# Kernel optimization log

Measured on AMD Instinct MI355X. Metric: run time of the kernel, lower is better.

The kernel has to match this reference:

```python
import jax, jax.numpy as jnp
import numpy as np

DIM = 512
A_HEADS = 8
C_HEADS = 4
DH = 64
EPS = 1e-5


def layer_norm(x, g, b):
    mu = jnp.mean(x, axis=-1, keepdims=True)
    var = jnp.var(x, axis=-1, keepdims=True)
    return (x - mu) * jax.lax.rsqrt(var + EPS) * g + b


def setup_inputs() -> dict:
    key = jax.random.key(0)
    ks = jax.random.split(key, 8)
    inner_a = A_HEADS * DH  # 512
    inner_c = C_HEADS * DH  # 256
    s = 0.02
    return {
        "x": jax.random.normal(ks[0], (4, 192, DIM), dtype=jnp.float32),
        # Attention branch params
        "ln1_g": jnp.ones((DIM,), jnp.float32),
        "ln1_b": jnp.zeros((DIM,), jnp.float32),
        "Wqkv": jax.random.normal(ks[1], (DIM, 3 * inner_a), jnp.float32) * s,
        "Wo": jax.random.normal(ks[2], (inner_a, DIM), jnp.float32) * s,
        "bo": jnp.zeros((DIM,), jnp.float32),
        # Trittention branch params
        "ln2_g": jnp.ones((DIM,), jnp.float32),
        "ln2_b": jnp.zeros((DIM,), jnp.float32),
        "Wabcde": jax.random.normal(ks[3], (DIM, 5 * inner_c), jnp.float32) * s,
        "babcde": jnp.zeros((5 * inner_c,), jnp.float32),
        "Wp": jax.random.normal(ks[4], (inner_c, DIM), jnp.float32) * s,
        "bp": jnp.zeros((DIM,), jnp.float32),
    }


def _attention(x, ln_g, ln_b, Wqkv, Wo, bo):
    B, T, _ = x.shape
    xn = layer_norm(x, ln_g, ln_b)
    qkv = xn @ Wqkv  # [B,T,3*H*D]
    q, k, v = jnp.split(qkv, 3, axis=-1)
    def heads(t):
        return t.reshape(B, T, A_HEADS, DH).transpose(0, 2, 1, 3)  # [B,H,T,D]
    q, k, v = heads(q), heads(k), heads(v)
    scale = DH ** -0.5
    dots = jnp.einsum('bhqd,bhkd->bhqk', q, k) * scale
    attn = jax.nn.softmax(dots, axis=-1)
    out = jnp.einsum('bhqk,bhkd->bhqd', attn, v)
    out = out.transpose(0, 2, 1, 3).reshape(B, T, A_HEADS * DH)
    return out @ Wo + bo


def _trittention(x, ln_g, ln_b, Wabcde, babcde, Wp, bp):
    B, T, _ = x.shape
    xn = layer_norm(x, ln_g, ln_b)
    proj = xn @ Wabcde + babcde  # [B,T,5*H*D]
    a, b_, c, d_, e = jnp.split(proj, 5, axis=-1)
    def heads(t):
        return t.reshape(B, T, C_HEADS, DH)  # [B,T,H,D]
    a, b_, c, d_, e = heads(a), heads(b_), heads(c), heads(d_), heads(e)
    # cubic score: [B,H,S,T,Q]
    score = jnp.einsum('bshd,bthd,bqhd->bhstq', a, b_, c) / DH
    # softmax over joint (s,t) for each query q
    score = score.transpose(0, 1, 4, 2, 3).reshape(B, C_HEADS, T, T * T)
    attn = jax.nn.softmax(score, axis=-1).reshape(B, C_HEADS, T, T, T)
    z = (jnp.einsum('bhqst,bshd->bhqd', attn, d_)
         + jnp.einsum('bhqst,bthd->bhqd', attn, e))
    z = z.transpose(0, 2, 1, 3).reshape(B, T, C_HEADS * DH)
    return z @ Wp + bp


def reference(x, ln1_g, ln1_b, Wqkv, Wo, bo, ln2_g, ln2_b, Wabcde, babcde, Wp, bp):
    return (_attention(x, ln1_g, ln1_b, Wqkv, Wo, bo)
            + _trittention(x, ln2_g, ln2_b, Wabcde, babcde, Wp, bp))
```

## Files before the change

kernel.cpp:

```cpp
#include <hip/hip_runtime.h>
#include <cstdint>


#define B_   4
#define T_   192
#define DIM_ 512
#define AH   8
#define CH   4

typedef unsigned short u16;
typedef unsigned int   u32;
typedef __attribute__((ext_vector_type(8))) short short8;
typedef __attribute__((ext_vector_type(4))) float floatx4;
typedef __attribute__((ext_vector_type(4))) int intx4;
typedef __attribute__((ext_vector_type(2))) float f32x2;
typedef __attribute__((ext_vector_type(8))) _Float16 half8;
typedef __attribute__((ext_vector_type(2))) _Float16 half2v;
typedef __attribute__((ext_vector_type(2))) __fp16 fp16x2;

union Frag  { intx4 i; short8 s; };
union FragH { intx4 i; half8 h; };

__device__ __forceinline__ floatx4 mfma16(Frag a, Frag b, floatx4 c) {
    return __builtin_amdgcn_mfma_f32_16x16x32_bf16(a.s, b.s, c, 0, 0, 0);
}
__device__ __forceinline__ floatx4 mfma16h(FragH a, FragH b, floatx4 c) {
    return __builtin_amdgcn_mfma_f32_16x16x32_f16(a.h, b.h, c, 0, 0, 0);
}

__device__ __forceinline__ float fexp2(float x) {
    return __builtin_amdgcn_exp2f(x);
}

__device__ __forceinline__ float wave_reduce_sum(float v) {
#pragma unroll
    for (int off = 32; off >= 1; off >>= 1)
        v += __shfl_xor(v, off, 64);
    return v;
}

__device__ __forceinline__ u32 pack_rne(float x, float y) {
    u32 ux = __float_as_uint(x);
    u32 uy = __float_as_uint(y);
    ux += 0x7fffu + ((ux >> 16) & 1u);
    uy += 0x7fffu + ((uy >> 16) & 1u);
    return (ux >> 16) | (uy & 0xffff0000u);
}
__device__ __forceinline__ u16 bf16_rne(float x) {
    u32 u = __float_as_uint(x);
    u += 0x7fffu + ((u >> 16) & 1u);
    return (u16)(u >> 16);
}
__device__ __forceinline__ float bf16f(u16 h) { return __uint_as_float(((u32)h) << 16); }

__device__ __forceinline__ u32 pack_f16(float x, float y) {
    union { fp16x2 h; u32 u; } cv;
    cv.h = __builtin_amdgcn_cvt_pkrtz(x, y);
    return cv.u;
}
__device__ __forceinline__ u32 mul_h2(u32 a, u32 b) {
    union { u32 u; half2v h; } ua, ub, uw;
    ua.u = a; ub.u = b;
    uw.h = ua.h * ub.h;
    return uw.u;
}

__device__ __forceinline__ Frag ld_frag8(const u16* p) {
    Frag f;
    uint2 a = *(const uint2*)p;
    uint2 b = *(const uint2*)(p + 4);
    f.i = (intx4){ (int)a.x, (int)a.y, (int)b.x, (int)b.y };
    return f;
}

#define LOG2E 1.44269504088896f

__global__ __launch_bounds__(256) void prep_kernel(
    const float* __restrict__ x,
    const float* __restrict__ g1, const float* __restrict__ b1,
    const float* __restrict__ g2, const float* __restrict__ b2,
    u16* __restrict__ x1h, u16* __restrict__ x2h,
    const float* __restrict__ Wqkv, u16* __restrict__ wqh,
    const float* __restrict__ Wab,  u16* __restrict__ wah,
    const float* __restrict__ Wo,   const float* __restrict__ Wp,
    u16* __restrict__ wofh, float* __restrict__ zero_base, float* __restrict__ outz)
{
    __shared__ union { float t[64][65]; float red[4][2]; } u;
    const int tid = threadIdx.x;
    {
        int gid = blockIdx.x * 256 + tid;
        if (gid < 294912) ((float4*)zero_base)[gid] = make_float4(0.f, 0.f, 0.f, 0.f);
        if (gid < 98304)  ((float4*)outz)[gid]      = make_float4(0.f, 0.f, 0.f, 0.f);
    }
    if (blockIdx.x < 768) {
        int row = blockIdx.x;
        const float2 v = ((const float2*)(x + (size_t)row * DIM_))[tid];
        float s  = v.x + v.y;
        float s2 = v.x * v.x + v.y * v.y;
        s  = wave_reduce_sum(s);
        s2 = wave_reduce_sum(s2);
        int w = tid >> 6;
        if ((tid & 63) == 0) { u.red[w][0] = s; u.red[w][1] = s2; }
        __syncthreads();
        float ts  = u.red[0][0] + u.red[1][0] + u.red[2][0] + u.red[3][0];
        float ts2 = u.red[0][1] + u.red[1][1] + u.red[2][1] + u.red[3][1];
        float mean = ts * (1.0f / DIM_);
        float var  = ts2 * (1.0f / DIM_) - mean * mean;
        float rstd = rsqrtf(var + 1e-5f);
        int c0 = tid * 2;
        float n0 = (v.x - mean) * rstd;
        float n1 = (v.y - mean) * rstd;
        float a0 = n0 * g1[c0] + b1[c0], a1 = n1 * g1[c0 + 1] + b1[c0 + 1];
        float c2 = n0 * g2[c0] + b2[c0], c3 = n1 * g2[c0 + 1] + b2[c0 + 1];
        size_t o = (size_t)row * 256 + tid;
        ((u32*)x1h)[o] = pack_rne(a0, a1);
        ((u32*)x2h)[o] = pack_rne(c2, c3);
        return;
    }
    int id = blockIdx.x - 768;
    const float* W; u16 *H; int K, N, Kout, kofs, tile;
    if (id < 192)      { W = Wqkv; H = wqh;  K = 512; N = 1536; Kout = 512; kofs = 0;   tile = id;       }
    else if (id < 352) { W = Wab;  H = wah;  K = 512; N = 1280; Kout = 512; kofs = 0;   tile = id - 192; }
    else if (id < 416) { W = Wo;   H = wofh; K = 512; N = 512;  Kout = 768; kofs = 0;   tile = id - 352; }
    else               { W = Wp;   H = wofh; K = 256; N = 512;  Kout = 768; kofs = 512; tile = id - 416; }
    int nx = N >> 6;
    int n0 = (tile % nx) * 64, k0 = (tile / nx) * 64;
    int rr = tid >> 4, c4 = (tid & 15) << 2;
#pragma unroll
    for (int p = 0; p < 4; ++p) {
        int row = rr + p * 16;
        float4 v = *(const float4*)(W + (size_t)(k0 + row) * N + n0 + c4);
        u.t[row][c4 + 0] = v.x; u.t[row][c4 + 1] = v.y;
        u.t[row][c4 + 2] = v.z; u.t[row][c4 + 3] = v.w;
    }
    __syncthreads();
#pragma unroll
    for (int p = 0; p < 4; ++p) {
        int n = rr + p * 16;
        u16 hi[4];
#pragma unroll
        for (int c = 0; c < 4; ++c)
            hi[c] = bf16_rne(u.t[c4 + c][n]);
        size_t o = (size_t)(n0 + n) * Kout + kofs + k0 + c4;
        *(uint2*)&H[o] = make_uint2((u32)hi[0] | ((u32)hi[1] << 16), (u32)hi[2] | ((u32)hi[3] << 16));
    }
}

__global__ __launch_bounds__(256) void gemm_dual(
    const u16* __restrict__ x1h, const u16* __restrict__ wqh,
    const u16* __restrict__ x2h, const u16* __restrict__ wah,
    const float* __restrict__ babcde,
    float* __restrict__ qkv, float* __restrict__ proj)
{
    __shared__ u16 As[64][68];
    __shared__ u16 Bs[64][68];
    const int tid = threadIdx.x;
    const int nb = blockIdx.x;
    const u16 *Ah, *BTh; const float* bias; float* C; int N, bn;
    if (nb < 24) { Ah = x1h; BTh = wqh; bias = nullptr; C = qkv;  N = 1536; bn = nb * 64; }
    else         { Ah = x2h; BTh = wah; bias = babcde; C = proj; N = 1280; bn = (nb - 24) * 64; }
    const int K = 512;
    const int bm = blockIdx.y * 64;
    const int lane = tid & 63, wave = tid >> 6;
    const int m16 = lane & 15, quad = lane >> 4;
    const int wm = (wave >> 1) * 32, wn = (wave & 1) * 32;
    const int r = tid >> 2, c16 = (tid & 3) * 16;

    floatx4 acc[2][2];
#pragma unroll
    for (int i = 0; i < 2; ++i)
#pragma unroll
        for (int j = 0; j < 2; ++j) acc[i][j] = (floatx4){0.f, 0.f, 0.f, 0.f};

    for (int k0 = 0; k0 < K; k0 += 64) {
        __syncthreads();
        {
            const u16* pa = x1h == Ah ? Ah + (size_t)(bm + r) * K + k0 + c16
                                      : Ah + (size_t)(bm + r) * K + k0 + c16;
            uint4 v0 = *(const uint4*)pa, v1 = *(const uint4*)(pa + 8);
            *(uint2*)&As[r][c16 + 0]  = make_uint2(v0.x, v0.y);
            *(uint2*)&As[r][c16 + 4]  = make_uint2(v0.z, v0.w);
            *(uint2*)&As[r][c16 + 8]  = make_uint2(v1.x, v1.y);
            *(uint2*)&As[r][c16 + 12] = make_uint2(v1.z, v1.w);
        }
        {
            const u16* pb = BTh + (size_t)(bn + r) * K + k0 + c16;
            uint4 v0 = *(const uint4*)pb, v1 = *(const uint4*)(pb + 8);
            *(uint2*)&Bs[r][c16 + 0]  = make_uint2(v0.x, v0.y);
            *(uint2*)&Bs[r][c16 + 4]  = make_uint2(v0.z, v0.w);
            *(uint2*)&Bs[r][c16 + 8]  = make_uint2(v1.x, v1.y);
            *(uint2*)&Bs[r][c16 + 12] = make_uint2(v1.z, v1.w);
        }
        __syncthreads();
#pragma unroll
        for (int ks = 0; ks < 2; ++ks) {
            const int ko = ks * 32 + quad * 8;
            Frag a0 = ld_frag8(&As[wm + m16][ko]);
            Frag a1 = ld_frag8(&As[wm + 16 + m16][ko]);
            Frag b0 = ld_frag8(&Bs[wn + m16][ko]);
            Frag b1 = ld_frag8(&Bs[wn + 16 + m16][ko]);
            acc[0][0] = mfma16(a0, b0, acc[0][0]);
            acc[0][1] = mfma16(a0, b1, acc[0][1]);
            acc[1][0] = mfma16(a1, b0, acc[1][0]);
            acc[1][1] = mfma16(a1, b1, acc[1][1]);
        }
    }
#pragma unroll
    for (int i = 0; i < 2; ++i)
#pragma unroll
        for (int rr = 0; rr < 4; ++rr) {
            int m = bm + wm + i * 16 + quad * 4 + rr;
#pragma unroll
            for (int j = 0; j < 2; ++j) {
                int n = bn + wn + j * 16 + m16;
                float v = acc[i][j][rr];
                if (bias) v += bias[n];
                C[(size_t)m * N + n] = v;
            }
        }
}

__global__ __launch_bounds__(256, 3) void attn_tritt(
    const float* __restrict__ qkv, const float* __restrict__ proj,
    u16* __restrict__ aoh, float* __restrict__ rs1, float* __restrict__ rt1)
{
    __shared__ union {
        struct {
            union { u16 Ks[96][68]; u16 P[64][100]; } kp;
            u16 Vt[64][100];
        } at;
        struct {
            u32 a_lds[48 * 36];
            u32 b_lds[48 * 36];
            float rs_lds[48][33];
            float rt_lds[48][33];
        } tr;
    } S;
    const int tid = threadIdx.x;
    const int lane = tid & 63, wave = tid >> 6;
    const int m16 = lane & 15, quad = lane >> 4;

    if (blockIdx.x < 96) {
        const int ab = blockIdx.x;
        const int b = ab / 24, rem = ab % 24;
        const int h = rem / 3, qt3 = rem % 3;
        const int qg = wave;
        const size_t base = (size_t)(b * T_) * 1536 + h * 64;

        Frag qf0, qf1;
        {
            const float s = 0.125f * LOG2E;
            const float* qp = qkv + base + (size_t)(qt3 * 64 + qg * 16 + m16) * 1536 + quad * 8;
            float4 u0 = *(const float4*)qp;
            float4 u1 = *(const float4*)(qp + 4);
            float4 u2 = *(const float4*)(qp + 32);
            float4 u3 = *(const float4*)(qp + 36);
            qf0.i = (intx4){ (int)pack_rne(u0.x * s, u0.y * s), (int)pack_rne(u0.z * s, u0.w * s),
                             (int)pack_rne(u1.x * s, u1.y * s), (int)pack_rne(u1.z * s, u1.w * s) };
            qf1.i = (intx4){ (int)pack_rne(u2.x * s, u2.y * s), (int)pack_rne(u2.z * s, u2.w * s),
                             (int)pack_rne(u3.x * s, u3.y * s), (int)pack_rne(u3.z * s, u3.w * s) };
        }

        float rsum[4] = {0.f, 0.f, 0.f, 0.f};
        floatx4 acco[4];
#pragma unroll
        for (int dt = 0; dt < 4; ++dt) acco[dt] = (floatx4){0.f, 0.f, 0.f, 0.f};

        for (int p = 0; p < 2; ++p) {
            if (p) __syncthreads();
            for (int i = tid; i < 96 * 16; i += 256) {
                int row = i >> 4, c4 = (i & 15) << 2;
                const float* kp = qkv + base + (size_t)(p * 96 + row) * 1536 + 512 + c4;
                float4 kv = *(const float4*)kp;
                *(uint2*)&S.at.kp.Ks[row][c4] = make_uint2(pack_rne(kv.x, kv.y), pack_rne(kv.z, kv.w));
                float4 vv = *(const float4*)(qkv + base + (size_t)(p * 96 + row) * 1536 + 1024 + c4);
                S.at.Vt[c4 + 0][row] = bf16_rne(vv.x);
                S.at.Vt[c4 + 1][row] = bf16_rne(vv.y);
                S.at.Vt[c4 + 2][row] = bf16_rne(vv.z);
                S.at.Vt[c4 + 3][row] = bf16_rne(vv.w);
            }
            __syncthreads();

            float ev[6][4];
#pragma unroll
            for (int tt = 0; tt < 6; ++tt) {
                Frag kb0 = ld_frag8(&S.at.kp.Ks[tt * 16 + m16][quad * 8]);
                Frag kb1 = ld_frag8(&S.at.kp.Ks[tt * 16 + m16][32 + quad * 8]);
                floatx4 accs = (floatx4){0.f, 0.f, 0.f, 0.f};
                accs = mfma16(qf0, kb0, accs);
                accs = mfma16(qf1, kb1, accs);
#pragma unroll
                for (int rr = 0; rr < 4; ++rr) {
                    float e = fexp2(accs[rr]);
                    ev[tt][rr] = e;
                    rsum[rr] += e;
                }
            }
            __syncthreads();
#pragma unroll
            for (int tt = 0; tt < 6; ++tt)
#pragma unroll
                for (int rr = 0; rr < 4; ++rr)
                    S.at.kp.P[qg * 16 + quad * 4 + rr][tt * 16 + m16] = bf16_rne(ev[tt][rr]);
#pragma unroll
            for (int ts = 0; ts < 3; ++ts) {
                Frag pf = ld_frag8(&S.at.kp.P[qg * 16 + m16][ts * 32 + quad * 8]);
#pragma unroll
                for (int dt = 0; dt < 4; ++dt) {
                    Frag vf = ld_frag8(&S.at.Vt[dt * 16 + m16][ts * 32 + quad * 8]);
                    acco[dt] = mfma16(pf, vf, acco[dt]);
                }
            }
        }

        float rinv[4];
#pragma unroll
        for (int rr = 0; rr < 4; ++rr) {
            float v = rsum[rr];
            v += __shfl_xor(v, 1, 64);
            v += __shfl_xor(v, 2, 64);
            v += __shfl_xor(v, 4, 64);
            v += __shfl_xor(v, 8, 64);
            rinv[rr] = 1.0f / v;
        }
#pragma unroll
        for (int dt = 0; dt < 4; ++dt)
#pragma unroll
            for (int rr = 0; rr < 4; ++rr) {
                float o = acco[dt][rr] * rinv[rr];
                size_t idx = (size_t)(b * T_ + qt3 * 64 + qg * 16 + quad * 4 + rr) * 512
                           + h * 64 + dt * 16 + m16;
                aoh[idx] = bf16_rne(o);
            }
        return;
    }

    const int t2 = blockIdx.x - 96;
    const int xx = t2 % 96;
    const int h = (t2 / 96) % CH;
    const int b = t2 / (96 * CH);
    const int qt = xx >> 4;
    const int sc = (xx >> 2) & 3;
    const int tc = xx & 3;
    const int q0 = qt * 32, s0 = sc * 48, t0 = tc * 48;
    const int bh = b * CH + h;
    const size_t rowbase = (size_t)(b * T_) * 1280 + h * 64;
    const float kA = 0.015625f * LOG2E;

    for (int i = tid; i < 48 * 32; i += 256) {
        int row = i >> 5, cp = i & 31;
        const float2 va = *(const float2*)(proj + rowbase + (size_t)(s0 + row) * 1280 + 0 + cp * 2);
        S.tr.a_lds[row * 36 + cp] = pack_f16(va.x * kA, va.y * kA);
        const float2 vb = *(const float2*)(proj + rowbase + (size_t)(t0 + row) * 1280 + 256 + cp * 2);
        S.tr.b_lds[row * 36 + cp] = pack_f16(vb.x, vb.y);
    }

    FragH cf[2][2];
#pragma unroll
    for (int jq = 0; jq < 2; ++jq) {
        const float* cp = proj + rowbase + (size_t)(q0 + jq * 16 + m16) * 1280 + 512 + quad * 8;
        float4 u0 = *(const float4*)(cp);
        float4 u1 = *(const float4*)(cp + 4);
        float4 u2 = *(const float4*)(cp + 32);
        float4 u3 = *(const float4*)(cp + 36);
        cf[jq][0].i = (intx4){ (int)pack_f16(u0.x, u0.y), (int)pack_f16(u0.z, u0.w),
                               (int)pack_f16(u1.x, u1.y), (int)pack_f16(u1.z, u1.w) };
        cf[jq][1].i = (intx4){ (int)pack_f16(u2.x, u2.y), (int)pack_f16(u2.z, u2.w),
                               (int)pack_f16(u3.x, u3.y), (int)pack_f16(u3.z, u3.w) };
    }
    __syncthreads();

    float rt_acc[3][4][2] = {};

    for (int si = 0; si < 12; ++si) {
        const int srow = wave * 12 + si;
        const intx4 av0 = *(const intx4*)(S.tr.a_lds + srow * 36 + quad * 4);
        const intx4 av1 = *(const intx4*)(S.tr.a_lds + srow * 36 + 16 + quad * 4);
        float rs_s[2] = {0.f, 0.f};
#pragma unroll
        for (int tt = 0; tt < 3; ++tt) {
            const u32* bp = S.tr.b_lds + (tt * 16 + m16) * 36;
            intx4 bv0 = *(const intx4*)(bp + quad * 4);
            intx4 bv1 = *(const intx4*)(bp + 16 + quad * 4);
            FragH w0, w1;
#pragma unroll
            for (int j = 0; j < 4; ++j) {
                w0.i[j] = (int)mul_h2((u32)av0[j], (u32)bv0[j]);
                w1.i[j] = (int)mul_h2((u32)av1[j], (u32)bv1[j]);
            }
#pragma unroll
            for (int jq = 0; jq < 2; ++jq) {
                floatx4 acc = (floatx4){0.f, 0.f, 0.f, 0.f};
                acc = mfma16h(w0, cf[jq][0], acc);
                acc = mfma16h(w1, cf[jq][1], acc);
#pragma unroll
                for (int rr = 0; rr < 4; ++rr) {
                    float e = fexp2(acc[rr]);
                    rt_acc[tt][rr][jq] += e;
                    rs_s[jq] += e;
                }
            }
        }
#pragma unroll
        for (int jq = 0; jq < 2; ++jq) {
            float v = rs_s[jq];
            v += __shfl_xor(v, 16, 64);
            v += __shfl_xor(v, 32, 64);
            if (lane < 16) S.tr.rs_lds[srow][jq * 16 + m16] = v;
        }
    }

    __syncthreads();
    for (int w = 0; w < 4; ++w) {
        if (wave == w) {
#pragma unroll
            for (int tt = 0; tt < 3; ++tt)
#pragma unroll
                for (int rr = 0; rr < 4; ++rr) {
                    int t = tt * 16 + quad * 4 + rr;
#pragma unroll
                    for (int jq = 0; jq < 2; ++jq) {
                        if (w == 0) S.tr.rt_lds[t][jq * 16 + m16] = rt_acc[tt][rr][jq];
                        else        S.tr.rt_lds[t][jq * 16 + m16] += rt_acc[tt][rr][jq];
                    }
                }
        }
        __syncthreads();
    }
    for (int i = tid; i < 32 * 48; i += 256) {
        int qq = i / 48, ss = i - qq * 48;
        unsafeAtomicAdd(&rs1[((size_t)bh * T_ + q0 + qq) * T_ + s0 + ss], S.tr.rs_lds[ss][qq]);
    }
    for (int i = tid; i < 32 * 48; i += 256) {
        int qq = i / 48, t3 = i - qq * 48;
        unsafeAtomicAdd(&rt1[((size_t)bh * T_ + q0 + qq) * T_ + t0 + t3], S.tr.rt_lds[t3][qq]);
    }
}

__global__ __launch_bounds__(256) void finale(
    const u16* __restrict__ aoh, const float* __restrict__ rs1, const float* __restrict__ rt1,
    const float* __restrict__ proj, const u16* __restrict__ wofh,
    const float* __restrict__ bo, const float* __restrict__ bp,
    float* __restrict__ out)
{
    __shared__ union {
        struct { u16 As[32][68]; u16 Bs[64][68]; } A;
        struct { u16 Am[2][32][68]; u16 Bs[64][68]; float zred[32][9]; float Zl[32]; } B;
    } S;
    const int tid = threadIdx.x;
    const int lane = tid & 63, wave = tid >> 6;
    const int m16 = lane & 15, quad = lane >> 4;

    if (blockIdx.x < 192) {
        const int bn = (blockIdx.x & 7) * 64, bm = (blockIdx.x >> 3) * 32;
        const int wm = (wave >> 1) * 16, wn = (wave & 1) * 32;
        const int ra = tid >> 3, c8 = (tid & 7) * 8;
        const int rb = tid >> 2, c16 = (tid & 3) * 16;

        floatx4 acc[2];
        acc[0] = (floatx4){0.f, 0.f, 0.f, 0.f};
        acc[1] = (floatx4){0.f, 0.f, 0.f, 0.f};

        for (int k0 = 0; k0 < 512; k0 += 64) {
            __syncthreads();
            {
                const u16* pah = aoh + (size_t)(bm + ra) * 512 + k0 + c8;
                uint4 v = *(const uint4*)pah;
                *(uint2*)&S.A.As[ra][c8 + 0] = make_uint2(v.x, v.y);
                *(uint2*)&S.A.As[ra][c8 + 4] = make_uint2(v.z, v.w);
            }
            {
                const u16* pb = wofh + (size_t)(bn + rb) * 768 + k0 + c16;
                uint4 v0 = *(const uint4*)pb, v1 = *(const uint4*)(pb + 8);
                *(uint2*)&S.A.Bs[rb][c16 + 0]  = make_uint2(v0.x, v0.y);
                *(uint2*)&S.A.Bs[rb][c16 + 4]  = make_uint2(v0.z, v0.w);
                *(uint2*)&S.A.Bs[rb][c16 + 8]  = make_uint2(v1.x, v1.y);
                *(uint2*)&S.A.Bs[rb][c16 + 12] = make_uint2(v1.z, v1.w);
            }
            __syncthreads();
#pragma unroll
            for (int ks = 0; ks < 2; ++ks) {
                const int ko = ks * 32 + quad * 8;
                Frag ah = ld_frag8(&S.A.As[wm + m16][ko]);
                Frag b0 = ld_frag8(&S.A.Bs[wn + m16][ko]);
                Frag b1 = ld_frag8(&S.A.Bs[wn + 16 + m16][ko]);
                acc[0] = mfma16(ah, b0, acc[0]);
                acc[1] = mfma16(ah, b1, acc[1]);
            }
        }
#pragma unroll
        for (int rr = 0; rr < 4; ++rr) {
            int m = bm + wm + quad * 4 + rr;
#pragma unroll
            for (int j = 0; j < 2; ++j) {
                int n = bn + wn + j * 16 + m16;
                unsafeAtomicAdd(&out[(size_t)m * 512 + n], acc[j][rr] + bo[n] + bp[n]);
            }
        }
        return;
    }

    const int blockB = blockIdx.x - 192;
    const int mt = blockB % 6, bh = blockB / 6;
    const int b = bh >> 2, h = bh & 3;
    const int q0 = mt * 32;
    const int wm = (wave >> 1) * 16, wn = (wave & 1) * 32;
    const int ra = tid >> 3, c8 = (tid & 7) * 8;
    const int sl = tid >> 2, d4b = (tid & 3) * 4;

    float zacc = 0.f;
    floatx4 acc[2];
    acc[0] = (floatx4){0.f, 0.f, 0.f, 0.f};
    acc[1] = (floatx4){0.f, 0.f, 0.f, 0.f};

    for (int k0 = 0; k0 < 384; k0 += 64) {
        __syncthreads();
        {
            float g[8];
            if (k0 < 192) {
                const float* p = rs1 + ((size_t)bh * T_ + q0 + ra) * T_ + k0 + c8;
                float4 v0 = *(const float4*)(p);
                float4 v1 = *(const float4*)(p + 4);
                g[0] = v0.x; g[1] = v0.y; g[2] = v0.z; g[3] = v0.w;
                g[4] = v1.x; g[5] = v1.y; g[6] = v1.z; g[7] = v1.w;
                zacc += ((g[0] + g[1]) + (g[2] + g[3])) + ((g[4] + g[5]) + (g[6] + g[7]));
            } else {
                const float* p = rt1 + ((size_t)bh * T_ + q0 + ra) * T_ + (k0 - 192) + c8;
                float4 v0 = *(const float4*)(p);
                float4 v1 = *(const float4*)(p + 4);
                g[0] = v0.x; g[1] = v0.y; g[2] = v0.z; g[3] = v0.w;
                g[4] = v1.x; g[5] = v1.y; g[6] = v1.z; g[7] = v1.w;
            }
#pragma unroll
            for (int i = 0; i < 8; ++i) {
                u16 hi = bf16_rne(g[i]);
                S.B.Am[0][ra][c8 + i] = hi;
                S.B.Am[1][ra][c8 + i] = bf16_rne(g[i] - bf16f(hi));
            }
        }
        {
            const int colbase = (k0 < 192 ? 768 : 1024) + h * 64;
            const int s0 = (k0 < 192 ? k0 : k0 - 192);
#pragma unroll
            for (int i = 0; i < 4; ++i) {
                int dd = d4b + i * 16;
                float4 v = *(const float4*)(proj + (size_t)(b * T_ + s0 + sl) * 1280 + colbase + dd);
                S.B.Bs[dd + 0][sl] = bf16_rne(v.x);
                S.B.Bs[dd + 1][sl] = bf16_rne(v.y);
                S.B.Bs[dd + 2][sl] = bf16_rne(v.z);
                S.B.Bs[dd + 3][sl] = bf16_rne(v.w);
            }
        }
        __syncthreads();
#pragma unroll
        for (int ks = 0; ks < 2; ++ks) {
            const int ko = ks * 32 + quad * 8;
            Frag gh = ld_frag8(&S.B.Am[0][wm + m16][ko]);
            Frag gl = ld_frag8(&S.B.Am[1][wm + m16][ko]);
            Frag d0 = ld_frag8(&S.B.Bs[wn + m16][ko]);
            Frag d1 = ld_frag8(&S.B.Bs[wn + 16 + m16][ko]);
            acc[0] = mfma16(gh, d0, acc[0]);
            acc[0] = mfma16(gl, d0, acc[0]);
            acc[1] = mfma16(gh, d1, acc[1]);
            acc[1] = mfma16(gl, d1, acc[1]);
        }
    }
    S.B.zred[ra][tid & 7] = zacc;
    __syncthreads();
    if (tid < 32) {
        float s = ((S.B.zred[tid][0] + S.B.zred[tid][1]) + (S.B.zred[tid][2] + S.B.zred[tid][3]))
                + ((S.B.zred[tid][4] + S.B.zred[tid][5]) + (S.B.zred[tid][6] + S.B.zred[tid][7]));
        S.B.Zl[tid] = 1.0f / s;
    }
    __syncthreads();
    {
        float zv[2][4];
#pragma unroll
        for (int j = 0; j < 2; ++j)
#pragma unroll
            for (int rr = 0; rr < 4; ++rr) {
                int m = wm + quad * 4 + rr;
                zv[j][rr] = acc[j][rr] * S.B.Zl[m];
            }
        __syncthreads();
#pragma unroll
        for (int j = 0; j < 2; ++j)
#pragma unroll
            for (int rr = 0; rr < 4; ++rr) {
                int m = wm + quad * 4 + rr;
                int d = wn + j * 16 + m16;
                S.B.Am[0][m][d] = bf16_rne(zv[j][rr]);
            }
    }
    __syncthreads();
#pragma unroll
    for (int t = 0; t < 8; ++t) {
        const int n0 = wave * 128 + t * 16;
        Frag bf0 = ld_frag8(&wofh[(size_t)(n0 + m16) * 768 + 512 + h * 64 + quad * 8]);
        Frag bf1 = ld_frag8(&wofh[(size_t)(n0 + m16) * 768 + 512 + h * 64 + 32 + quad * 8]);
#pragma unroll
        for (int qi = 0; qi < 2; ++qi) {
            Frag za = ld_frag8(&S.B.Am[0][qi * 16 + m16][quad * 8]);
            Frag zb = ld_frag8(&S.B.Am[0][qi * 16 + m16][32 + quad * 8]);
            floatx4 ac = (floatx4){0.f, 0.f, 0.f, 0.f};
            ac = mfma16(za, bf0, ac);
            ac = mfma16(zb, bf1, ac);
#pragma unroll
            for (int rr = 0; rr < 4; ++rr) {
                int m = b * T_ + q0 + qi * 16 + quad * 4 + rr;
                unsafeAtomicAdd(&out[(size_t)m * 512 + n0 + m16], ac[rr]);
            }
        }
    }
}

extern "C" void kernel_launch(void* const* d_in, const int* in_sizes, int n_in,
                              void* d_out, int out_size, void* d_ws, size_t ws_size,
                              hipStream_t stream)
{
    const float* x      = (const float*)d_in[0];
    const float* ln1_g  = (const float*)d_in[1];
    const float* ln1_b  = (const float*)d_in[2];
    const float* Wqkv   = (const float*)d_in[3];
    const float* Wo     = (const float*)d_in[4];
    const float* bo     = (const float*)d_in[5];
    const float* ln2_g  = (const float*)d_in[6];
    const float* ln2_b  = (const float*)d_in[7];
    const float* Wabcde = (const float*)d_in[8];
    const float* babcde = (const float*)d_in[9];
    const float* Wp     = (const float*)d_in[10];
    const float* bp     = (const float*)d_in[11];
    float* out = (float*)d_out;

    float* ws   = (float*)d_ws;
    float* proj = ws;
    u16* wofh   = (u16*)(ws + 983040);
    u16* aoh    = (u16*)(ws + 1179648);
    float* qkv  = ws + 1376256;
    u16* x1h    = (u16*)(ws + 2555904);
    u16* x2h    = (u16*)(ws + 2752512);
    u16* wqh    = (u16*)(ws + 2949120);
    u16* wah    = (u16*)(ws + 3342336);
    float* rs1  = ws + 3670016;
    float* rt1  = ws + 4259840;

    prep_kernel<<<1216, 256, 0, stream>>>(x, ln1_g, ln1_b, ln2_g, ln2_b,
                                          x1h, x2h,
                                          Wqkv, wqh, Wabcde, wah,
                                          Wo, Wp, wofh, rs1, out);
    gemm_dual<<<dim3(44, 12), 256, 0, stream>>>(x1h, wqh, x2h, wah,
                                                babcde, qkv, proj);
    attn_tritt<<<96 + 1536, 256, 0, stream>>>(qkv, proj, aoh, rs1, rt1);
    finale<<<288, 256, 0, stream>>>(aoh, rs1, rt1, proj, wofh, bo, bp, out);
}
```

Before: 138.8 us.

## Fuse attention output projection into attention blocks via per-head atomic accumulation

Each attention block now writes its normalized per-head output to shared memory and multiplies it directly by its 64-column slice of Wo, atomically adding partial results (plus biases from head 0) into the output. This removes the bf16 attention-output buffer round trip and the 192 output-projection GEMM blocks from the final kernel, which shrinks to the trittention part only. In exchange it adds eight-way atomic contention per output element, an extra Wo read per head block, and more work on the 96 attention blocks, which may lengthen the attention kernel's critical path.

```diff
diff --git a/kernel.cpp b/kernel.cpp
--- a/kernel.cpp
+++ b/kernel.cpp
@@ -175,8 +175,7 @@
     for (int k0 = 0; k0 < K; k0 += 64) {
         __syncthreads();
         {
-            const u16* pa = x1h == Ah ? Ah + (size_t)(bm + r) * K + k0 + c16
-                                      : Ah + (size_t)(bm + r) * K + k0 + c16;
+            const u16* pa = Ah + (size_t)(bm + r) * K + k0 + c16;
             uint4 v0 = *(const uint4*)pa, v1 = *(const uint4*)(pa + 8);
             *(uint2*)&As[r][c16 + 0]  = make_uint2(v0.x, v0.y);
             *(uint2*)&As[r][c16 + 4]  = make_uint2(v0.z, v0.w);
@@ -222,11 +221,14 @@
 
 __global__ __launch_bounds__(256, 3) void attn_tritt(
     const float* __restrict__ qkv, const float* __restrict__ proj,
-    u16* __restrict__ aoh, float* __restrict__ rs1, float* __restrict__ rt1)
+    const u16* __restrict__ wofh,
+    const float* __restrict__ bo, const float* __restrict__ bp,
+    float* __restrict__ rs1, float* __restrict__ rt1,
+    float* __restrict__ out)
 {
     __shared__ union {
         struct {
-            union { u16 Ks[96][68]; u16 P[64][100]; } kp;
+            union { u16 Ks[96][68]; u16 P[64][100]; u16 oz[64][68]; } kp;
             u16 Vt[64][100];
         } at;
         struct {
@@ -323,15 +325,39 @@
             v += __shfl_xor(v, 8, 64);
             rinv[rr] = 1.0f / v;
         }
+        __syncthreads();
 #pragma unroll
         for (int dt = 0; dt < 4; ++dt)
 #pragma unroll
             for (int rr = 0; rr < 4; ++rr) {
                 float o = acco[dt][rr] * rinv[rr];
-                size_t idx = (size_t)(b * T_ + qt3 * 64 + qg * 16 + quad * 4 + rr) * 512
-                           + h * 64 + dt * 16 + m16;
-                aoh[idx] = bf16_rne(o);
-            }
+                S.at.kp.oz[qg * 16 + quad * 4 + rr][dt * 16 + m16] = bf16_rne(o);
+            }
+        __syncthreads();
+        const int brow = b * T_ + qt3 * 64;
+        const bool addb = (h == 0);
+#pragma unroll
+        for (int t = 0; t < 8; ++t) {
+            const int n0 = wave * 128 + t * 16;
+            Frag wo0 = ld_frag8(&wofh[(size_t)(n0 + m16) * 768 + h * 64 + quad * 8]);
+            Frag wo1 = ld_frag8(&wofh[(size_t)(n0 + m16) * 768 + h * 64 + 32 + quad * 8]);
+#pragma unroll
+            for (int qi = 0; qi < 4; ++qi) {
+                Frag oa = ld_frag8(&S.at.kp.oz[qi * 16 + m16][quad * 8]);
+                Frag ob = ld_frag8(&S.at.kp.oz[qi * 16 + m16][32 + quad * 8]);
+                floatx4 ac = (floatx4){0.f, 0.f, 0.f, 0.f};
+                ac = mfma16(oa, wo0, ac);
+                ac = mfma16(ob, wo1, ac);
+#pragma unroll
+                for (int rr = 0; rr < 4; ++rr) {
+                    int m = brow + qi * 16 + quad * 4 + rr;
+                    int n = n0 + m16;
+                    float v = ac[rr];
+                    if (addb) v += bo[n] + bp[n];
+                    unsafeAtomicAdd(&out[(size_t)m * 512 + n], v);
+                }
+            }
+        }
         return;
     }
 
@@ -379,9 +405,9 @@
         float rs_s[2] = {0.f, 0.f};
 #pragma unroll
         for (int tt = 0; tt < 3; ++tt) {
-            const u32* bp = S.tr.b_lds + (tt * 16 + m16) * 36;
-            intx4 bv0 = *(const intx4*)(bp + quad * 4);
-            intx4 bv1 = *(const intx4*)(bp + 16 + quad * 4);
+            const u32* bp2 = S.tr.b_lds + (tt * 16 + m16) * 36;
+            intx4 bv0 = *(const intx4*)(bp2 + quad * 4);
+            intx4 bv1 = *(const intx4*)(bp2 + 16 + quad * 4);
             FragH w0, w1;
 #pragma unroll
             for (int j = 0; j < 4; ++j) {
@@ -438,69 +464,16 @@
 }
 
 __global__ __launch_bounds__(256) void finale(
-    const u16* __restrict__ aoh, const float* __restrict__ rs1, const float* __restrict__ rt1,
+    const float* __restrict__ rs1, const float* __restrict__ rt1,
     const float* __restrict__ proj, const u16* __restrict__ wofh,
-    const float* __restrict__ bo, const float* __restrict__ bp,
     float* __restrict__ out)
 {
-    __shared__ union {
-        struct { u16 As[32][68]; u16 Bs[64][68]; } A;
-        struct { u16 Am[2][32][68]; u16 Bs[64][68]; float zred[32][9]; float Zl[32]; } B;
-    } S;
+    __shared__ struct { u16 Am[2][32][68]; u16 Bs[64][68]; float zred[32][9]; float Zl[32]; } S;
     const int tid = threadIdx.x;
     const int lane = tid & 63, wave = tid >> 6;
     const int m16 = lane & 15, quad = lane >> 4;
 
-    if (blockIdx.x < 192) {
-        const int bn = (blockIdx.x & 7) * 64, bm = (blockIdx.x >> 3) * 32;
-        const int wm = (wave >> 1) * 16, wn = (wave & 1) * 32;
-        const int ra = tid >> 3, c8 = (tid & 7) * 8;
-        const int rb = tid >> 2, c16 = (tid & 3) * 16;
-
-        floatx4 acc[2];
-        acc[0] = (floatx4){0.f, 0.f, 0.f, 0.f};
-        acc[1] = (floatx4){0.f, 0.f, 0.f, 0.f};
-
-        for (int k0 = 0; k0 < 512; k0 += 64) {
-            __syncthreads();
-            {
-                const u16* pah = aoh + (size_t)(bm + ra) * 512 + k0 + c8;
-                uint4 v = *(const uint4*)pah;
-                *(uint2*)&S.A.As[ra][c8 + 0] = make_uint2(v.x, v.y);
-                *(uint2*)&S.A.As[ra][c8 + 4] = make_uint2(v.z, v.w);
-            }
-            {
-                const u16* pb = wofh + (size_t)(bn + rb) * 768 + k0 + c16;
-                uint4 v0 = *(const uint4*)pb, v1 = *(const uint4*)(pb + 8);
-                *(uint2*)&S.A.Bs[rb][c16 + 0]  = make_uint2(v0.x, v0.y);
-                *(uint2*)&S.A.Bs[rb][c16 + 4]  = make_uint2(v0.z, v0.w);
-                *(uint2*)&S.A.Bs[rb][c16 + 8]  = make_uint2(v1.x, v1.y);
-                *(uint2*)&S.A.Bs[rb][c16 + 12] = make_uint2(v1.z, v1.w);
-            }
-            __syncthreads();
-#pragma unroll
-            for (int ks = 0; ks < 2; ++ks) {
-                const int ko = ks * 32 + quad * 8;
-                Frag ah = ld_frag8(&S.A.As[wm + m16][ko]);
-                Frag b0 = ld_frag8(&S.A.Bs[wn + m16][ko]);
-                Frag b1 = ld_frag8(&S.A.Bs[wn + 16 + m16][ko]);
-                acc[0] = mfma16(ah, b0, acc[0]);
-                acc[1] = mfma16(ah, b1, acc[1]);
-            }
-        }
-#pragma unroll
-        for (int rr = 0; rr < 4; ++rr) {
-            int m = bm + wm + quad * 4 + rr;
-#pragma unroll
-            for (int j = 0; j < 2; ++j) {
-                int n = bn + wn + j * 16 + m16;
-                unsafeAtomicAdd(&out[(size_t)m * 512 + n], acc[j][rr] + bo[n] + bp[n]);
-            }
-        }
-        return;
-    }
-
-    const int blockB = blockIdx.x - 192;
+    const int blockB = blockIdx.x;
     const int mt = blockB % 6, bh = blockB / 6;
     const int b = bh >> 2, h = bh & 3;
     const int q0 = mt * 32;
@@ -534,8 +507,8 @@
 #pragma unroll
             for (int i = 0; i < 8; ++i) {
                 u16 hi = bf16_rne(g[i]);
-                S.B.Am[0][ra][c8 + i] = hi;
-                S.B.Am[1][ra][c8 + i] = bf16_rne(g[i] - bf16f(hi));
+                S.Am[0][ra][c8 + i] = hi;
+                S.Am[1][ra][c8 + i] = bf16_rne(g[i] - bf16f(hi));
             }
         }
         {
@@ -545,32 +518,32 @@
             for (int i = 0; i < 4; ++i) {
                 int dd = d4b + i * 16;
                 float4 v = *(const float4*)(proj + (size_t)(b * T_ + s0 + sl) * 1280 + colbase + dd);
-                S.B.Bs[dd + 0][sl] = bf16_rne(v.x);
-                S.B.Bs[dd + 1][sl] = bf16_rne(v.y);
-                S.B.Bs[dd + 2][sl] = bf16_rne(v.z);
-                S.B.Bs[dd + 3][sl] = bf16_rne(v.w);
+                S.Bs[dd + 0][sl] = bf16_rne(v.x);
+                S.Bs[dd + 1][sl] = bf16_rne(v.y);
+                S.Bs[dd + 2][sl] = bf16_rne(v.z);
+                S.Bs[dd + 3][sl] = bf16_rne(v.w);
             }
         }
         __syncthreads();
 #pragma unroll
         for (int ks = 0; ks < 2; ++ks) {
             const int ko = ks * 32 + quad * 8;
-            Frag gh = ld_frag8(&S.B.Am[0][wm + m16][ko]);
-            Frag gl = ld_frag8(&S.B.Am[1][wm + m16][ko]);
-            Frag d0 = ld_frag8(&S.B.Bs[wn + m16][ko]);
-            Frag d1 = ld_frag8(&S.B.Bs[wn + 16 + m16][ko]);
+            Frag gh = ld_frag8(&S.Am[0][wm + m16][ko]);
+            Frag gl = ld_frag8(&S.Am[1][wm + m16][ko]);
+            Frag d0 = ld_frag8(&S.Bs[wn + m16][ko]);
+            Frag d1 = ld_frag8(&S.Bs[wn + 16 + m16][ko]);
             acc[0] = mfma16(gh, d0, acc[0]);
             acc[0] = mfma16(gl, d0, acc[0]);
             acc[1] = mfma16(gh, d1, acc[1]);
             acc[1] = mfma16(gl, d1, acc[1]);
         }
     }
-    S.B.zred[ra][tid & 7] = zacc;
+    S.zred[ra][tid & 7] = zacc;
     __syncthreads();
     if (tid < 32) {
-        float s = ((S.B.zred[tid][0] + S.B.zred[tid][1]) + (S.B.zred[tid][2] + S.B.zred[tid][3]))
-                + ((S.B.zred[tid][4] + S.B.zred[tid][5]) + (S.B.zred[tid][6] + S.B.zred[tid][7]));
-        S.B.Zl[tid] = 1.0f / s;
+        float s = ((S.zred[tid][0] + S.zred[tid][1]) + (S.zred[tid][2] + S.zred[tid][3]))
+                + ((S.zred[tid][4] + S.zred[tid][5]) + (S.zred[tid][6] + S.zred[tid][7]));
+        S.Zl[tid] = 1.0f / s;
     }
     __syncthreads();
     {
@@ -580,7 +553,7 @@
 #pragma unroll
             for (int rr = 0; rr < 4; ++rr) {
                 int m = wm + quad * 4 + rr;
-                zv[j][rr] = acc[j][rr] * S.B.Zl[m];
+                zv[j][rr] = acc[j][rr] * S.Zl[m];
             }
         __syncthreads();
 #pragma unroll
@@ -589,7 +562,7 @@
             for (int rr = 0; rr < 4; ++rr) {
                 int m = wm + quad * 4 + rr;
                 int d = wn + j * 16 + m16;
-                S.B.Am[0][m][d] = bf16_rne(zv[j][rr]);
+                S.Am[0][m][d] = bf16_rne(zv[j][rr]);
             }
     }
     __syncthreads();
@@ -600,8 +573,8 @@
         Frag bf1 = ld_frag8(&wofh[(size_t)(n0 + m16) * 768 + 512 + h * 64 + 32 + quad * 8]);
 #pragma unroll
         for (int qi = 0; qi < 2; ++qi) {
-            Frag za = ld_frag8(&S.B.Am[0][qi * 16 + m16][quad * 8]);
-            Frag zb = ld_frag8(&S.B.Am[0][qi * 16 + m16][32 + quad * 8]);
+            Frag za = ld_frag8(&S.Am[0][qi * 16 + m16][quad * 8]);
+            Frag zb = ld_frag8(&S.Am[0][qi * 16 + m16][32 + quad * 8]);
             floatx4 ac = (floatx4){0.f, 0.f, 0.f, 0.f};
             ac = mfma16(za, bf0, ac);
             ac = mfma16(zb, bf1, ac);
@@ -635,7 +608,6 @@
     float* ws   = (float*)d_ws;
     float* proj = ws;
     u16* wofh   = (u16*)(ws + 983040);
-    u16* aoh    = (u16*)(ws + 1179648);
     float* qkv  = ws + 1376256;
     u16* x1h    = (u16*)(ws + 2555904);
     u16* x2h    = (u16*)(ws + 2752512);
@@ -650,6 +622,6 @@
                                           Wo, Wp, wofh, rs1, out);
     gemm_dual<<<dim3(44, 12), 256, 0, stream>>>(x1h, wqh, x2h, wah,
                                                 babcde, qkv, proj);
-    attn_tritt<<<96 + 1536, 256, 0, stream>>>(qkv, proj, aoh, rs1, rt1);
-    finale<<<288, 256, 0, stream>>>(aoh, rs1, rt1, proj, wofh, bo, bp, out);
-}
+    attn_tritt<<<96 + 1536, 256, 0, stream>>>(qkv, proj, wofh, bo, bp, rs1, rt1, out);
+    finale<<<96, 256, 0, stream>>>(rs1, rt1, proj, wofh, out);
+}
```

New measurement: 181.4 us. 1.31x slower.
